# Performance work log

Hardware: AMD Instinct MI355X
Metric: run time of the kernel (lower is better)

The kernel has to match this reference:

```python
import jax, jax.numpy as jnp
import numpy as np

N = 100_000   # atoms
B = 10_000    # building blocks
E = 320_000   # edges (bb <- atom)
D = 256       # embed_dim
H = 8         # heads
HD = D // H   # head_dim = 32
DIST = 64     # gaussian dist embed dim
MAX_R = 10.0


def setup_inputs() -> dict:
    key = jax.random.key(0)
    ks = jax.random.split(key, 10)
    atom_feats = jax.random.normal(ks[0], (N, D), jnp.float32)
    coords = jax.random.normal(ks[1], (N, 3), jnp.float32) * 3.0
    bb_vec = jnp.sort(jax.random.randint(ks[2], (N,), 0, B, jnp.int32))
    src = jax.random.randint(ks[3], (E,), 0, N, jnp.int32)
    tgt = jax.random.randint(ks[4], (E,), 0, B, jnp.int32)
    # linear params, [in, out] layout (x @ W + b)
    Wq = jax.random.normal(ks[5], (D, D), jnp.float32) / np.sqrt(D)
    Wk = jax.random.normal(ks[6], (D + DIST, D), jnp.float32) / np.sqrt(D + DIST)
    Wv = jax.random.normal(ks[7], (D + DIST, D), jnp.float32) / np.sqrt(D + DIST)
    Wo = jax.random.normal(ks[8], (D, D), jnp.float32) / np.sqrt(D)
    bq = jnp.zeros((D,), jnp.float32)
    bk = jnp.zeros((D,), jnp.float32)
    bv = jnp.zeros((D,), jnp.float32)
    bo = jnp.zeros((D,), jnp.float32)
    return dict(atom_feats=atom_feats, coords=coords, Wq=Wq, bq=bq, Wk=Wk, bk=bk,
                Wv=Wv, bv=bv, Wo=Wo, bo=bo, bb_vec=bb_vec, src=src, tgt=tgt)


def _gaussian_smearing(dist):
    offsets = jnp.linspace(0.0, MAX_R, DIST)            # [DIST]
    coeff = -0.5 / (offsets[1] - offsets[0]) ** 2
    return jnp.exp(coeff * (dist[:, None] - offsets) ** 2)  # [E, DIST]


def reference(atom_feats, coords, Wq, bq, Wk, bk, Wv, bv, Wo, bo, bb_vec, src, tgt):
    # building-block centers: mean coords, summed feats per bb
    counts = jax.ops.segment_sum(jnp.ones((N,), coords.dtype), bb_vec, num_segments=B)
    bb_center_pos = jax.ops.segment_sum(coords, bb_vec, num_segments=B)
    bb_center_pos = bb_center_pos / jnp.maximum(counts, 1.0)[:, None]       # [B, 3]
    bb_center_feats = jax.ops.segment_sum(atom_feats, bb_vec, num_segments=B)  # [B, D]

    # per-edge distance embedding
    edge_vec = coords[src] - bb_center_pos[tgt]                             # [E, 3]
    dist = jnp.sqrt(jnp.sum(edge_vec * edge_vec, axis=-1))                  # [E]
    edge_dist_embed = _gaussian_smearing(dist)                              # [E, DIST]

    # QKV
    q = (bb_center_feats @ Wq + bq).reshape(B, H, HD)                       # [B, H, HD]
    atom_input = jnp.concatenate([atom_feats[src], edge_dist_embed], -1)    # [E, D+DIST]
    k = (atom_input @ Wk + bk).reshape(E, H, HD)
    v = (atom_input @ Wv + bv).reshape(E, H, HD)

    # per-edge attention logits + segment softmax over tgt
    attn = jnp.einsum('ehc,ehc->eh', q[tgt], k) / np.sqrt(HD)               # [E, H]
    seg_max = jax.ops.segment_max(attn, tgt, num_segments=B)                # [B, H]
    ex = jnp.exp(attn - seg_max[tgt])
    denom = jax.ops.segment_sum(ex, tgt, num_segments=B)                    # [B, H]
    attn = ex / (denom[tgt] + 1e-16)

    # weighted scatter-sum of messages
    msg = attn[..., None] * v                                               # [E, H, HD]
    out = jax.ops.segment_sum(msg, tgt, num_segments=B).reshape(B, D)       # [B, D]
    return out @ Wo + bo
```

## Files before the change

kernel.cpp:

```cpp
#include <hip/hip_runtime.h>
#include <math.h>

#define N_ATOMS 100000
#define B_BB    10000
#define E_EDGES 320000
#define D_DIM   256
#define NHEAD   8
#define NDIST   64

#define DELTA   (10.0f/63.0f)
#define GCOEFF  (-0.5f/(DELTA*DELTA))
#define QKSCALE 0.17677669529663687f

__global__ void k_offsets(const int* __restrict__ bb_vec, int* __restrict__ atom_off,
                          int* __restrict__ edge_cnt) {
  int b = blockIdx.x * 256 + threadIdx.x;
  if (b <= B_BB) {
    int lo = 0, hi = N_ATOMS;
    while (lo < hi) { int mid = (lo + hi) >> 1; if (bb_vec[mid] < b) lo = mid + 1; else hi = mid; }
    atom_off[b] = lo;
  }
  if (b < B_BB) edge_cnt[b] = 0;
}

__global__ __launch_bounds__(256) void k_bb_centers(
    const float* __restrict__ af, const float* __restrict__ coords,
    const int* __restrict__ atom_off, float* __restrict__ bbF, float* __restrict__ bb_pos) {
  int t = threadIdx.x;
  for (int b = blockIdx.x; b < B_BB; b += gridDim.x) {
    int s = atom_off[b], e = atom_off[b + 1];
    float acc = 0.f;
    for (int a = s; a < e; a++) acc += af[(size_t)a * D_DIM + t];
    bbF[(size_t)b * D_DIM + t] = acc;
    if (t < 3) {
      float c = 0.f;
      for (int a = s; a < e; a++) c += coords[(size_t)a * 3 + t];
      float cnt = (float)(e - s);
      bb_pos[b * 4 + t] = c / fmaxf(cnt, 1.0f);
    }
  }
}

__global__ __launch_bounds__(256) void k_gemm256(
    const float* __restrict__ A, const float* __restrict__ W,
    const float* __restrict__ bias, float* __restrict__ C, int M) {
  __shared__ __align__(16) float As[16][68];
  __shared__ __align__(16) float Ws[16][64];
  int tid = threadIdx.x;
  int tx = tid & 15, ty = tid >> 4;
  int row0 = blockIdx.x * 64, col0 = blockIdx.y * 64;
  float acc[4][4] = {};
  for (int k0 = 0; k0 < 256; k0 += 16) {
    {
      int r = tid >> 2;
      int c = (tid & 3) * 4;
      int row = row0 + r;
      float4 v = make_float4(0.f, 0.f, 0.f, 0.f);
      if (row < M) v = *(const float4*)&A[(size_t)row * 256 + k0 + c];
      As[c + 0][r] = v.x; As[c + 1][r] = v.y; As[c + 2][r] = v.z; As[c + 3][r] = v.w;
    }
    {
      int r = tid >> 4;
      int c = (tid & 15) * 4;
      float4 v = *(const float4*)&W[(size_t)(k0 + r) * 256 + col0 + c];
      *(float4*)&Ws[r][c] = v;
    }
    __syncthreads();
#pragma unroll
    for (int kk = 0; kk < 16; kk++) {
      float4 a = *(const float4*)&As[kk][ty * 4];
      float4 b = *(const float4*)&Ws[kk][tx * 4];
      float av[4] = {a.x, a.y, a.z, a.w};
      float bv4[4] = {b.x, b.y, b.z, b.w};
#pragma unroll
      for (int i = 0; i < 4; i++)
#pragma unroll
        for (int j = 0; j < 4; j++) acc[i][j] += av[i] * bv4[j];
    }
    __syncthreads();
  }
#pragma unroll
  for (int i = 0; i < 4; i++) {
    int row = row0 + ty * 4 + i;
    if (row < M) {
      int col = col0 + tx * 4;
      float4 r = make_float4(acc[i][0] + bias[col + 0], acc[i][1] + bias[col + 1],
                             acc[i][2] + bias[col + 2], acc[i][3] + bias[col + 3]);
      *(float4*)&C[(size_t)row * 256 + col] = r;
    }
  }
}

__global__ void k_hist(const int* __restrict__ tgt, int* __restrict__ edge_cnt) {
  int e = blockIdx.x * 256 + threadIdx.x;
  if (e < E_EDGES) atomicAdd(&edge_cnt[tgt[e]], 1);
}

__global__ __launch_bounds__(1024) void k_scan(
    const int* __restrict__ edge_cnt, int* __restrict__ edge_start, int* __restrict__ cursor) {
  __shared__ int ssum[1024];
  int tid = threadIdx.x;
  int base = tid * 10;
  int v[10]; int s = 0;
#pragma unroll
  for (int k = 0; k < 10; k++) { int i = base + k; v[k] = (i < B_BB) ? edge_cnt[i] : 0; s += v[k]; }
  ssum[tid] = s;
  __syncthreads();
  for (int off = 1; off < 1024; off <<= 1) {
    int t = (tid >= off) ? ssum[tid - off] : 0;
    __syncthreads();
    ssum[tid] += t;
    __syncthreads();
  }
  int excl = ssum[tid] - s;
#pragma unroll
  for (int k = 0; k < 10; k++) {
    int i = base + k;
    if (i < B_BB) { edge_start[i] = excl; cursor[i] = excl; }
    excl += v[k];
  }
  if (tid == 1023) edge_start[B_BB] = E_EDGES;
}

__global__ void k_fill(const int* __restrict__ src, const int* __restrict__ tgt,
                       const float* __restrict__ coords, const float* __restrict__ bb_pos,
                       int* __restrict__ cursor, int* __restrict__ src_sorted,
                       float* __restrict__ dist_sorted) {
  int e = blockIdx.x * 256 + threadIdx.x;
  if (e >= E_EDGES) return;
  int b = tgt[e], a = src[e];
  int pos = atomicAdd(&cursor[b], 1);
  float dx = coords[a * 3 + 0] - bb_pos[b * 4 + 0];
  float dy = coords[a * 3 + 1] - bb_pos[b * 4 + 1];
  float dz = coords[a * 3 + 2] - bb_pos[b * 4 + 2];
  src_sorted[pos] = a;
  dist_sorted[pos] = sqrtf(dx * dx + dy * dy + dz * dz);
}

__global__ __launch_bounds__(256) void k_wt(
    const float* __restrict__ q, const float* __restrict__ Wk, float* __restrict__ wt) {
  __shared__ __align__(16) float As[32][132];
  __shared__ __align__(16) float Bs[32][68];
  int tid = threadIdx.x;
  int b0 = blockIdx.x * 128;
  int i0 = blockIdx.y * 64;
  int h  = blockIdx.z;
  {
    int r = tid >> 1, c0 = (tid & 1) * 16;
    int row = b0 + r;
    const float* qp = q + (size_t)row * 256 + h * 32 + c0;
#pragma unroll
    for (int jj = 0; jj < 4; ++jj) {
      float4 v = make_float4(0.f, 0.f, 0.f, 0.f);
      if (row < B_BB) v = *(const float4*)(qp + 4 * jj);
      As[c0 + 4*jj + 0][r] = v.x; As[c0 + 4*jj + 1][r] = v.y;
      As[c0 + 4*jj + 2][r] = v.z; As[c0 + 4*jj + 3][r] = v.w;
    }
  }
  {
    int r = tid >> 2, c0 = (tid & 3) * 8;
    const float* wp = Wk + (size_t)(i0 + r) * 256 + h * 32 + c0;
#pragma unroll
    for (int jj = 0; jj < 2; ++jj) {
      float4 v = *(const float4*)(wp + 4 * jj);
      Bs[c0 + 4*jj + 0][r] = v.x; Bs[c0 + 4*jj + 1][r] = v.y;
      Bs[c0 + 4*jj + 2][r] = v.z; Bs[c0 + 4*jj + 3][r] = v.w;
    }
  }
  __syncthreads();
  int tx = tid & 15, ty = tid >> 4;
  float acc[8][4] = {};
#pragma unroll
  for (int kk = 0; kk < 32; ++kk) {
    float4 a0 = *(const float4*)&As[kk][ty * 8];
    float4 a1 = *(const float4*)&As[kk][ty * 8 + 4];
    float4 b4 = *(const float4*)&Bs[kk][tx * 4];
    float av[8] = {a0.x, a0.y, a0.z, a0.w, a1.x, a1.y, a1.z, a1.w};
    float bv4[4] = {b4.x, b4.y, b4.z, b4.w};
#pragma unroll
    for (int i = 0; i < 8; ++i)
#pragma unroll
      for (int j = 0; j < 4; ++j) acc[i][j] += av[i] * bv4[j];
  }
#pragma unroll
  for (int i = 0; i < 8; ++i) {
    int row = b0 + ty * 8 + i;
    if (row < B_BB) {
      float4 o = make_float4(acc[i][0] * QKSCALE, acc[i][1] * QKSCALE,
                             acc[i][2] * QKSCALE, acc[i][3] * QKSCALE);
      *(float4*)&wt[(size_t)row * 2560 + h * 320 + i0 + tx * 4] = o;
    }
  }
}

__global__ __launch_bounds__(256) void k_attn(
    const float* __restrict__ af, float* __restrict__ wtS,
    const int* __restrict__ edge_start, const int* __restrict__ src_sorted,
    const float* __restrict__ dist_sorted, float* __restrict__ wsum) {
  int tid = threadIdx.x;
  int lane = tid & 63;
  int wv = tid >> 6;
  int h0 = 2 * wv, h1 = 2 * wv + 1;
  int g = lane >> 4;
  int sub = lane & 15;
  int b = blockIdx.x;

  int s0 = edge_start[b], e1 = edge_start[b + 1];
  float* wtb = wtS + (size_t)b * 2560;
  const float* wr0 = wtb + h0 * 320;
  const float* wr1 = wtb + h1 * 320;

  float W0[16], W1[16], wd0[4], wd1[4];
#pragma unroll
  for (int j = 0; j < 4; ++j) {
    float4 t0 = *(const float4*)(wr0 + sub * 16 + 4 * j);
    float4 t1 = *(const float4*)(wr1 + sub * 16 + 4 * j);
    W0[4*j+0] = t0.x; W0[4*j+1] = t0.y; W0[4*j+2] = t0.z; W0[4*j+3] = t0.w;
    W1[4*j+0] = t1.x; W1[4*j+1] = t1.y; W1[4*j+2] = t1.z; W1[4*j+3] = t1.w;
  }
#pragma unroll
  for (int j = 0; j < 4; ++j) { wd0[j] = wr0[256 + sub + 16*j]; wd1[j] = wr1[256 + sub + 16*j]; }

  float l0 = 0.f, l1 = 0.f;
  float S0r[16] = {}, S1r[16] = {};
  float sd0[4] = {}, sd1[4] = {};

  if (s0 < e1) {
    int e1m1 = e1 - 1;
    int i0 = min(s0 + g, e1m1);
    int aC = src_sorted[i0];
    float dC = dist_sorted[i0];
    int i1 = min(s0 + 4 + g, e1m1);
    int aN = src_sorted[i1];
    float dN = dist_sorted[i1];
    const float4* crow = (const float4*)(af + (size_t)aC * 256 + sub * 16);
    float4 A0 = crow[0], A1 = crow[1], A2 = crow[2], A3 = crow[3];

    for (int eb = s0; eb < e1; eb += 4) {
      int i2 = min(eb + 8 + g, e1m1);
      int aN2 = src_sorted[i2];
      float dN2 = dist_sorted[i2];
      const float4* nrow = (const float4*)(af + (size_t)aN * 256 + sub * 16);
      float4 P0 = nrow[0], P1 = nrow[1], P2 = nrow[2], P3 = nrow[3];

      float Ar[16];
      Ar[0]=A0.x; Ar[1]=A0.y; Ar[2]=A0.z; Ar[3]=A0.w;
      Ar[4]=A1.x; Ar[5]=A1.y; Ar[6]=A1.z; Ar[7]=A1.w;
      Ar[8]=A2.x; Ar[9]=A2.y; Ar[10]=A2.z; Ar[11]=A2.w;
      Ar[12]=A3.x; Ar[13]=A3.y; Ar[14]=A3.z; Ar[15]=A3.w;
      float emb[4];
#pragma unroll
      for (int j = 0; j < 4; ++j) {
        float dd = dC - (float)(sub + 16 * j) * DELTA;
        emb[j] = __expf(GCOEFF * dd * dd);
      }
      float p0 = 0.f, p1 = 0.f;
#pragma unroll
      for (int c = 0; c < 16; ++c) { p0 += Ar[c] * W0[c]; p1 += Ar[c] * W1[c]; }
#pragma unroll
      for (int j = 0; j < 4; ++j) { p0 += emb[j] * wd0[j]; p1 += emb[j] * wd1[j]; }
#pragma unroll
      for (int off = 8; off > 0; off >>= 1) {
        p0 += __shfl_xor(p0, off);
        p1 += __shfl_xor(p1, off);
      }
      float w0 = __expf(p0), w1 = __expf(p1);
      if (eb + g >= e1) { w0 = 0.f; w1 = 0.f; }
      l0 += w0; l1 += w1;
#pragma unroll
      for (int c = 0; c < 16; ++c) {
        S0r[c] = fmaf(w0, Ar[c], S0r[c]);
        S1r[c] = fmaf(w1, Ar[c], S1r[c]);
      }
#pragma unroll
      for (int j = 0; j < 4; ++j) {
        sd0[j] = fmaf(w0, emb[j], sd0[j]);
        sd1[j] = fmaf(w1, emb[j], sd1[j]);
      }

      A0 = P0; A1 = P1; A2 = P2; A3 = P3;
      dC = dN;
      aN = aN2; dN = dN2;
    }
  }

#pragma unroll
  for (int off = 16; off <= 32; off <<= 1) {
    l0 += __shfl_xor(l0, off);
    l1 += __shfl_xor(l1, off);
#pragma unroll
    for (int c = 0; c < 16; ++c) {
      S0r[c] += __shfl_xor(S0r[c], off);
      S1r[c] += __shfl_xor(S1r[c], off);
    }
#pragma unroll
    for (int j = 0; j < 4; ++j) {
      sd0[j] += __shfl_xor(sd0[j], off);
      sd1[j] += __shfl_xor(sd1[j], off);
    }
  }

  float inv0 = 1.0f / (l0 + 1e-16f), inv1 = 1.0f / (l1 + 1e-16f);
  if (g == 0) {
#pragma unroll
    for (int j = 0; j < 4; ++j) {
      float4 o0 = make_float4(S0r[4*j+0]*inv0, S0r[4*j+1]*inv0, S0r[4*j+2]*inv0, S0r[4*j+3]*inv0);
      float4 o1 = make_float4(S1r[4*j+0]*inv1, S1r[4*j+1]*inv1, S1r[4*j+2]*inv1, S1r[4*j+3]*inv1);
      *(float4*)(wtb + h0 * 320 + sub * 16 + 4 * j) = o0;
      *(float4*)(wtb + h1 * 320 + sub * 16 + 4 * j) = o1;
    }
#pragma unroll
    for (int j = 0; j < 4; ++j) {
      wtb[h0 * 320 + 256 + sub + 16 * j] = sd0[j] * inv0;
      wtb[h1 * 320 + 256 + sub + 16 * j] = sd1[j] * inv1;
    }
    if (sub == 0) {
      wsum[b * 8 + h0] = l0 * inv0;
      wsum[b * 8 + h1] = l1 * inv1;
    }
  }
}

__global__ __launch_bounds__(256) void k_out_head(
    const float* __restrict__ Sf, const float* __restrict__ Wv,
    const float* __restrict__ bv, const float* __restrict__ wsum,
    float* __restrict__ out_pre) {
  __shared__ __align__(16) float As[32][132];
  __shared__ __align__(16) float Bs[32][36];
  int tid = threadIdx.x;
  int b0 = blockIdx.x * 128;
  int h  = blockIdx.y;
  int tx = tid & 7, ty = tid >> 3;
  float acc[4][4] = {};
  for (int k0 = 0; k0 < 320; k0 += 32) {
    {
      int r = tid >> 1, c0 = (tid & 1) * 16;
      int row = b0 + r;
      const float* sp = Sf + (size_t)row * 2560 + h * 320 + k0 + c0;
#pragma unroll
      for (int jj = 0; jj < 4; ++jj) {
        float4 v = make_float4(0.f, 0.f, 0.f, 0.f);
        if (row < B_BB) v = *(const float4*)(sp + 4 * jj);
        As[c0 + 4*jj + 0][r] = v.x; As[c0 + 4*jj + 1][r] = v.y;
        As[c0 + 4*jj + 2][r] = v.z; As[c0 + 4*jj + 3][r] = v.w;
      }
    }
    {
      int r = tid >> 3, c0 = (tid & 7) * 4;
      float4 v = *(const float4*)&Wv[(size_t)(k0 + r) * 256 + h * 32 + c0];
      *(float4*)&Bs[r][c0] = v;
    }
    __syncthreads();
#pragma unroll
    for (int kk = 0; kk < 32; ++kk) {
      float4 a4 = *(const float4*)&As[kk][ty * 4];
      float4 b4 = *(const float4*)&Bs[kk][tx * 4];
      float av[4] = {a4.x, a4.y, a4.z, a4.w};
      float bv4[4] = {b4.x, b4.y, b4.z, b4.w};
#pragma unroll
      for (int i = 0; i < 4; ++i)
#pragma unroll
        for (int j = 0; j < 4; ++j) acc[i][j] += av[i] * bv4[j];
    }
    __syncthreads();
  }
  float bvv[4];
#pragma unroll
  for (int j = 0; j < 4; ++j) bvv[j] = bv[h * 32 + tx * 4 + j];
#pragma unroll
  for (int i = 0; i < 4; ++i) {
    int row = b0 + ty * 4 + i;
    if (row < B_BB) {
      float ws = wsum[row * 8 + h];
      float4 o = make_float4(acc[i][0] + ws * bvv[0], acc[i][1] + ws * bvv[1],
                             acc[i][2] + ws * bvv[2], acc[i][3] + ws * bvv[3]);
      *(float4*)&out_pre[(size_t)row * 256 + h * 32 + tx * 4] = o;
    }
  }
}

extern "C" void kernel_launch(void* const* d_in, const int* in_sizes, int n_in,
                              void* d_out, int out_size, void* d_ws, size_t ws_size,
                              hipStream_t stream) {
  const float* af     = (const float*)d_in[0];
  const float* coords = (const float*)d_in[1];
  const float* Wq     = (const float*)d_in[2];
  const float* bq     = (const float*)d_in[3];
  const float* Wk     = (const float*)d_in[4];
  const float* bk     = (const float*)d_in[5];  (void)bk;
  const float* Wv     = (const float*)d_in[6];
  const float* bv     = (const float*)d_in[7];
  const float* Wo     = (const float*)d_in[8];
  const float* bo     = (const float*)d_in[9];
  const int* bb_vec   = (const int*)d_in[10];
  const int* src      = (const int*)d_in[11];
  const int* tgt      = (const int*)d_in[12];
  float* out = (float*)d_out;
  (void)in_sizes; (void)n_in; (void)out_size; (void)ws_size;

  char* ws = (char*)d_ws;
  size_t o = 0;
  auto alloc = [&](size_t bytes) { size_t r = o; o += (bytes + 255) & ~(size_t)255; return r; };
  int*   atom_off    = (int*)(ws + alloc((B_BB + 1) * 4));
  int*   edge_cnt    = (int*)(ws + alloc((size_t)B_BB * 4));
  int*   edge_start  = (int*)(ws + alloc((B_BB + 1) * 4));
  int*   cursor      = (int*)(ws + alloc((size_t)B_BB * 4));
  int*   src_sorted  = (int*)(ws + alloc((size_t)E_EDGES * 4));
  float* dist_sorted = (float*)(ws + alloc((size_t)E_EDGES * 4));
  float* bbF         = (float*)(ws + alloc((size_t)B_BB * 256 * 4));
  float* bb_pos      = (float*)(ws + alloc((size_t)B_BB * 4 * 4));
  float* q           = (float*)(ws + alloc((size_t)B_BB * 256 * 4));
  float* wtS         = (float*)(ws + alloc((size_t)B_BB * 2560 * 4));
  float* wsum        = (float*)(ws + alloc((size_t)B_BB * 8 * 4));
  float* out_pre     = (float*)(ws + alloc((size_t)B_BB * 256 * 4));

  k_offsets<<<(B_BB + 1 + 255) / 256, 256, 0, stream>>>(bb_vec, atom_off, edge_cnt);
  k_bb_centers<<<2560, 256, 0, stream>>>(af, coords, atom_off, bbF, bb_pos);
  k_hist<<<(E_EDGES + 255) / 256, 256, 0, stream>>>(tgt, edge_cnt);
  k_scan<<<1, 1024, 0, stream>>>(edge_cnt, edge_start, cursor);
  k_fill<<<(E_EDGES + 255) / 256, 256, 0, stream>>>(src, tgt, coords, bb_pos, cursor,
                                                    src_sorted, dist_sorted);
  k_gemm256<<<dim3((B_BB + 63) / 64, 4), 256, 0, stream>>>(bbF, Wq, bq, q, B_BB);
  k_wt<<<dim3((B_BB + 127) / 128, 5, 8), 256, 0, stream>>>(q, Wk, wtS);
  k_attn<<<B_BB, 256, 0, stream>>>(af, wtS, edge_start, src_sorted, dist_sorted, wsum);
  k_out_head<<<dim3((B_BB + 127) / 128, 8), 256, 0, stream>>>(wtS, Wv, bv, wsum, out_pre);
  k_gemm256<<<dim3((B_BB + 63) / 64, 4), 256, 0, stream>>>(out_pre, Wo, bo, out, B_BB);
}
```

Before: 563.1 us.

## Deepen attention prefetch, enlarge GEMM tiles, use wave-shuffle scan, split attn launch

The attention kernel now prefetches atom rows two edge-groups ahead instead of one, uses 32-bit float4 indexing, and sets a minimum of 3 blocks per CU through launch bounds, all to hide gather latency. The generic GEMM computes 128x64 tiles with 8x4 per thread instead of 64x64, halving its grid. The single-block scan uses wavefront shuffles instead of a 1024-step shared-memory Hillis-Steele loop with barriers. The attention launch is split into two half-size launches. Holding the deeper prefetch in registers competes with the occupancy target and may cause spills, and the extra launch adds overhead.

```diff
diff --git a/kernel.cpp b/kernel.cpp
--- a/kernel.cpp
+++ b/kernel.cpp
@@ -44,20 +44,25 @@
 __global__ __launch_bounds__(256) void k_gemm256(
     const float* __restrict__ A, const float* __restrict__ W,
     const float* __restrict__ bias, float* __restrict__ C, int M) {
-  __shared__ __align__(16) float As[16][68];
+  __shared__ __align__(16) float As[16][136];
   __shared__ __align__(16) float Ws[16][64];
   int tid = threadIdx.x;
   int tx = tid & 15, ty = tid >> 4;
-  int row0 = blockIdx.x * 64, col0 = blockIdx.y * 64;
-  float acc[4][4] = {};
+  int row0 = blockIdx.x * 128, col0 = blockIdx.y * 64;
+  float acc[8][4] = {};
   for (int k0 = 0; k0 < 256; k0 += 16) {
     {
-      int r = tid >> 2;
-      int c = (tid & 3) * 4;
+      int r = tid >> 1;
+      int kc = (tid & 1) * 8;
       int row = row0 + r;
-      float4 v = make_float4(0.f, 0.f, 0.f, 0.f);
-      if (row < M) v = *(const float4*)&A[(size_t)row * 256 + k0 + c];
-      As[c + 0][r] = v.x; As[c + 1][r] = v.y; As[c + 2][r] = v.z; As[c + 3][r] = v.w;
+      const float* ap = A + (size_t)row * 256 + k0 + kc;
+#pragma unroll
+      for (int jj = 0; jj < 2; ++jj) {
+        float4 v = make_float4(0.f, 0.f, 0.f, 0.f);
+        if (row < M) v = *(const float4*)(ap + 4 * jj);
+        As[kc + 4*jj + 0][r] = v.x; As[kc + 4*jj + 1][r] = v.y;
+        As[kc + 4*jj + 2][r] = v.z; As[kc + 4*jj + 3][r] = v.w;
+      }
     }
     {
       int r = tid >> 4;
@@ -68,20 +73,21 @@
     __syncthreads();
 #pragma unroll
     for (int kk = 0; kk < 16; kk++) {
-      float4 a = *(const float4*)&As[kk][ty * 4];
-      float4 b = *(const float4*)&Ws[kk][tx * 4];
-      float av[4] = {a.x, a.y, a.z, a.w};
-      float bv4[4] = {b.x, b.y, b.z, b.w};
-#pragma unroll
-      for (int i = 0; i < 4; i++)
+      float4 a0 = *(const float4*)&As[kk][ty * 8];
+      float4 a1 = *(const float4*)&As[kk][ty * 8 + 4];
+      float4 b4 = *(const float4*)&Ws[kk][tx * 4];
+      float av[8] = {a0.x, a0.y, a0.z, a0.w, a1.x, a1.y, a1.z, a1.w};
+      float bv4[4] = {b4.x, b4.y, b4.z, b4.w};
+#pragma unroll
+      for (int i = 0; i < 8; i++)
 #pragma unroll
         for (int j = 0; j < 4; j++) acc[i][j] += av[i] * bv4[j];
     }
     __syncthreads();
   }
 #pragma unroll
-  for (int i = 0; i < 4; i++) {
-    int row = row0 + ty * 4 + i;
+  for (int i = 0; i < 8; i++) {
+    int row = row0 + ty * 8 + i;
     if (row < M) {
       int col = col0 + tx * 4;
       float4 r = make_float4(acc[i][0] + bias[col + 0], acc[i][1] + bias[col + 1],
@@ -98,21 +104,33 @@
 
 __global__ __launch_bounds__(1024) void k_scan(
     const int* __restrict__ edge_cnt, int* __restrict__ edge_start, int* __restrict__ cursor) {
-  __shared__ int ssum[1024];
+  __shared__ int wtot[16];
   int tid = threadIdx.x;
+  int lane = tid & 63, w = tid >> 6;
   int base = tid * 10;
   int v[10]; int s = 0;
 #pragma unroll
   for (int k = 0; k < 10; k++) { int i = base + k; v[k] = (i < B_BB) ? edge_cnt[i] : 0; s += v[k]; }
-  ssum[tid] = s;
+  int x = s;
+#pragma unroll
+  for (int off = 1; off < 64; off <<= 1) {
+    int t = __shfl_up(x, off);
+    if (lane >= off) x += t;
+  }
+  if (lane == 63) wtot[w] = x;
   __syncthreads();
-  for (int off = 1; off < 1024; off <<= 1) {
-    int t = (tid >= off) ? ssum[tid - off] : 0;
-    __syncthreads();
-    ssum[tid] += t;
-    __syncthreads();
-  }
-  int excl = ssum[tid] - s;
+  if (w == 0 && lane < 16) {
+    int y = wtot[lane];
+#pragma unroll
+    for (int off = 1; off < 16; off <<= 1) {
+      int t = __shfl_up(y, off);
+      if (lane >= off) y += t;
+    }
+    wtot[lane] = y;
+  }
+  __syncthreads();
+  int wpre = (w == 0) ? 0 : wtot[w - 1];
+  int excl = wpre + x - s;
 #pragma unroll
   for (int k = 0; k < 10; k++) {
     int i = base + k;
@@ -193,17 +211,20 @@
   }
 }
 
-__global__ __launch_bounds__(256) void k_attn(
+__global__ __launch_bounds__(256, 3) void k_attn(
     const float* __restrict__ af, float* __restrict__ wtS,
     const int* __restrict__ edge_start, const int* __restrict__ src_sorted,
-    const float* __restrict__ dist_sorted, float* __restrict__ wsum) {
+    const float* __restrict__ dist_sorted, float* __restrict__ wsum,
+    int b_base) {
   int tid = threadIdx.x;
   int lane = tid & 63;
   int wv = tid >> 6;
   int h0 = 2 * wv, h1 = 2 * wv + 1;
   int g = lane >> 4;
   int sub = lane & 15;
-  int b = blockIdx.x;
+  int b = b_base + blockIdx.x;
+  const float4* afq = (const float4*)af;
+  unsigned subo = (unsigned)(sub * 4);
 
   int s0 = edge_start[b], e1 = edge_start[b + 1];
   float* wtb = wtS + (size_t)b * 2560;
@@ -228,20 +249,26 @@
   if (s0 < e1) {
     int e1m1 = e1 - 1;
     int i0 = min(s0 + g, e1m1);
-    int aC = src_sorted[i0];
+    int aA = src_sorted[i0];
     float dC = dist_sorted[i0];
     int i1 = min(s0 + 4 + g, e1m1);
-    int aN = src_sorted[i1];
+    int aP = src_sorted[i1];
     float dN = dist_sorted[i1];
-    const float4* crow = (const float4*)(af + (size_t)aC * 256 + sub * 16);
-    float4 A0 = crow[0], A1 = crow[1], A2 = crow[2], A3 = crow[3];
+    int i2 = min(s0 + 8 + g, e1m1);
+    int aR = src_sorted[i2];
+    float dNN = dist_sorted[i2];
+
+    const float4* arow = afq + ((unsigned)aA * 64u + subo);
+    float4 A0 = arow[0], A1 = arow[1], A2 = arow[2], A3 = arow[3];
+    const float4* prow = afq + ((unsigned)aP * 64u + subo);
+    float4 P0 = prow[0], P1 = prow[1], P2 = prow[2], P3 = prow[3];
 
     for (int eb = s0; eb < e1; eb += 4) {
-      int i2 = min(eb + 8 + g, e1m1);
-      int aN2 = src_sorted[i2];
-      float dN2 = dist_sorted[i2];
-      const float4* nrow = (const float4*)(af + (size_t)aN * 256 + sub * 16);
-      float4 P0 = nrow[0], P1 = nrow[1], P2 = nrow[2], P3 = nrow[3];
+      int i3 = min(eb + 12 + g, e1m1);
+      int aN3 = src_sorted[i3];
+      float dN3 = dist_sorted[i3];
+      const float4* rrow = afq + ((unsigned)aR * 64u + subo);
+      float4 R0 = rrow[0], R1 = rrow[1], R2 = rrow[2], R3 = rrow[3];
 
       float Ar[16];
       Ar[0]=A0.x; Ar[1]=A0.y; Ar[2]=A0.z; Ar[3]=A0.w;
@@ -279,8 +306,9 @@
       }
 
       A0 = P0; A1 = P1; A2 = P2; A3 = P3;
-      dC = dN;
-      aN = aN2; dN = dN2;
+      P0 = R0; P1 = R1; P2 = R2; P3 = R3;
+      dC = dN; dN = dNN; dNN = dN3;
+      aR = aN3;
     }
   }
 
@@ -420,9 +448,12 @@
   k_scan<<<1, 1024, 0, stream>>>(edge_cnt, edge_start, cursor);
   k_fill<<<(E_EDGES + 255) / 256, 256, 0, stream>>>(src, tgt, coords, bb_pos, cursor,
                                                     src_sorted, dist_sorted);
-  k_gemm256<<<dim3((B_BB + 63) / 64, 4), 256, 0, stream>>>(bbF, Wq, bq, q, B_BB);
+  k_gemm256<<<dim3((B_BB + 127) / 128, 4), 256, 0, stream>>>(bbF, Wq, bq, q, B_BB);
   k_wt<<<dim3((B_BB + 127) / 128, 5, 8), 256, 0, stream>>>(q, Wk, wtS);
-  k_attn<<<B_BB, 256, 0, stream>>>(af, wtS, edge_start, src_sorted, dist_sorted, wsum);
+  k_attn<<<B_BB / 2, 256, 0, stream>>>(af, wtS, edge_start, src_sorted, dist_sorted,
+                                       wsum, 0);
+  k_attn<<<B_BB / 2, 256, 0, stream>>>(af, wtS, edge_start, src_sorted, dist_sorted,
+                                       wsum, B_BB / 2);
   k_out_head<<<dim3((B_BB + 127) / 128, 8), 256, 0, stream>>>(wtS, Wv, bv, wsum, out_pre);
-  k_gemm256<<<dim3((B_BB + 63) / 64, 4), 256, 0, stream>>>(out_pre, Wo, bo, out, B_BB);
-}
+  k_gemm256<<<dim3((B_BB + 127) / 128, 4), 256, 0, stream>>>(out_pre, Wo, bo, out, B_BB);
+}
```

Result: slower. 607.2 us (+7.8%).
